# Kernel tuning notes

Hardware: AMD Instinct MI355X
Metric: run time of the kernel (lower is better)

The kernel has to match this reference:

```python
import jax, jax.numpy as jnp
import numpy as np

D_MODEL = 1024
N_HEAD = 16
D_K = D_MODEL // N_HEAD
B, S = 2, 2048
NEG = -1000000000.0


def setup_inputs() -> dict:
    key = jax.random.key(0)
    ks = jax.random.split(key, 9)
    inp = {
        "input_q": jax.random.normal(ks[0], (B, S, D_MODEL), dtype=jnp.float32),
        "input_k": jax.random.normal(ks[1], (B, S, D_MODEL), dtype=jnp.float32),
        "input_v": jax.random.normal(ks[2], (B, S, D_MODEL), dtype=jnp.float32),
        "mask": jax.random.randint(ks[3], (1, 1, S, S), 0, 2, dtype=jnp.int32),
        # parameters (Linear weights stored as [in, out] for x @ W)
        "w_q": jax.random.normal(ks[4], (D_MODEL, D_MODEL), dtype=jnp.float32) / np.sqrt(D_MODEL),
        "w_k": jax.random.normal(ks[5], (D_MODEL, D_MODEL), dtype=jnp.float32) / np.sqrt(D_MODEL),
        "w_v": jax.random.normal(ks[6], (D_MODEL, D_MODEL), dtype=jnp.float32) / np.sqrt(D_MODEL),
        "w_o": jax.random.normal(ks[7], (D_MODEL, D_MODEL), dtype=jnp.float32) / np.sqrt(D_MODEL),
        "b_o": jax.random.normal(ks[8], (D_MODEL,), dtype=jnp.float32) * 0.01,
    }
    return inp


def reference(input_q, input_k, input_v, mask, w_q, w_k, w_v, w_o, b_o):
    b = input_q.shape[0]
    # QKV projections -> [B, H, S, d_k]
    def split_heads(x):
        return x.reshape(b, -1, N_HEAD, D_K).transpose(0, 2, 1, 3)
    q = split_heads(input_q @ w_q)
    k = split_heads(input_k @ w_k)
    v = split_heads(input_v @ w_v)
    # naive attention: materialize [B, H, Sq, Sk] scores
    scores = jnp.einsum("bhqd,bhkd->bhqk", q, k) / jnp.sqrt(jnp.float32(D_K))
    scores = jnp.where(mask == 0, jnp.float32(NEG), scores)
    attn = jax.nn.softmax(scores, axis=-1)
    per_head = jnp.einsum("bhqk,bhkd->bhqd", attn, v)
    concat = per_head.transpose(0, 2, 1, 3).reshape(b, -1, N_HEAD * D_K)
    return concat @ w_o + b_o
```

## Files before the change

kernel.cpp:

```cpp
#include <hip/hip_runtime.h>
#include <hip/hip_bf16.h>

typedef _Float16 halfx8 __attribute__((ext_vector_type(8)));
typedef _Float16 halfx4 __attribute__((ext_vector_type(4)));
typedef _Float16 half2t __attribute__((ext_vector_type(2)));
typedef __fp16 fp16x2 __attribute__((ext_vector_type(2)));
typedef float floatx4 __attribute__((ext_vector_type(4)));

constexpr int S = 2048;
constexpr int DM = 1024;
constexpr int NH = 16;
constexpr int DK = 64;
constexpr int BATCH = 2;
constexpr int MROWS = 4096;
constexpr float QSCALE = 0.125f * 1.44269504088896340736f;

#if defined(__has_builtin)
#if __has_builtin(__builtin_amdgcn_fdot2)
#define HAVE_FDOT2 1
#endif
#endif

static __device__ inline half2t pack2(float a, float b) {
  return __builtin_bit_cast(half2t, __builtin_amdgcn_cvt_pkrtz(a, b));
}

static __device__ inline void load_lds16(const _Float16* g, _Float16* l) {
  __builtin_amdgcn_global_load_lds((const __attribute__((address_space(1))) void*)g,
                                   (__attribute__((address_space(3))) void*)l, 16, 0, 0);
}

__global__ void convert_w4(const float* __restrict__ w0, const float* __restrict__ w1,
                           const float* __restrict__ w2, const float* __restrict__ w3,
                           _Float16* __restrict__ o0, _Float16* __restrict__ o1,
                           _Float16* __restrict__ o2, _Float16* __restrict__ o3) {
  const float* w = (blockIdx.z == 0) ? w0 : (blockIdx.z == 1) ? w1 : (blockIdx.z == 2) ? w2 : w3;
  _Float16* wt = (blockIdx.z == 0) ? o0 : (blockIdx.z == 1) ? o1 : (blockIdx.z == 2) ? o2 : o3;
  __shared__ float tile[32][33];
  int n0 = blockIdx.x * 32, k0 = blockIdx.y * 32;
  int tx = threadIdx.x, ty = threadIdx.y;
#pragma unroll
  for (int i = 0; i < 4; ++i)
    tile[ty + i * 8][tx] = w[(k0 + ty + i * 8) * DM + n0 + tx];
  __syncthreads();
#pragma unroll
  for (int i = 0; i < 4; ++i)
    wt[(n0 + ty + i * 8) * DM + k0 + tx] = (_Float16)tile[tx][ty + i * 8];
}

__global__ void convert_in3(const float* __restrict__ a0, const float* __restrict__ a1,
                            const float* __restrict__ a2, _Float16* __restrict__ o0,
                            _Float16* __restrict__ o1, _Float16* __restrict__ o2) {
  const float* a = (blockIdx.z == 0) ? a0 : (blockIdx.z == 1) ? a1 : a2;
  _Float16* o = (blockIdx.z == 0) ? o0 : (blockIdx.z == 1) ? o1 : o2;
  size_t i = ((size_t)blockIdx.x * 256 + threadIdx.x) * 8;
  float4 va = *(const float4*)(a + i);
  float4 vb = *(const float4*)(a + i + 4);
  union { halfx8 v; _Float16 h[8]; } u;
  u.h[0] = (_Float16)va.x; u.h[1] = (_Float16)va.y;
  u.h[2] = (_Float16)va.z; u.h[3] = (_Float16)va.w;
  u.h[4] = (_Float16)vb.x; u.h[5] = (_Float16)vb.y;
  u.h[6] = (_Float16)vb.z; u.h[7] = (_Float16)vb.w;
  *(halfx8*)(o + i) = u.v;
}

__global__ void mask_swz(const int* __restrict__ m, _Float16* __restrict__ Mt) {
  int t = blockIdx.x * 256 + threadIdx.x;
  int j0 = (t & 1) * 8;
  int quad = (t >> 1) & 3;
  int q = (t >> 3) & (S - 1);
  int kt = t >> 14;
  const int* src = m + (size_t)q * S + kt * 64 + (j0 >> 2) * 16 + quad * 4;
  int4 a = *(const int4*)src;
  int4 b = *(const int4*)(src + 16);
  union { halfx8 v; _Float16 h[8]; } u;
  u.h[0] = (_Float16)(a.x != 0); u.h[1] = (_Float16)(a.y != 0);
  u.h[2] = (_Float16)(a.z != 0); u.h[3] = (_Float16)(a.w != 0);
  u.h[4] = (_Float16)(b.x != 0); u.h[5] = (_Float16)(b.y != 0);
  u.h[6] = (_Float16)(b.z != 0); u.h[7] = (_Float16)(b.w != 0);
  *(halfx8*)(Mt + (size_t)t * 8) = u.v;
}

__global__ __launch_bounds__(256) void qkv_gemm(const _Float16* __restrict__ xq,
                                                const _Float16* __restrict__ xk,
                                                const _Float16* __restrict__ xv,
                                                const _Float16* __restrict__ wqkv,
                                                _Float16* __restrict__ Qf,
                                                _Float16* __restrict__ Kf,
                                                _Float16* __restrict__ Vt) {
  __shared__ __align__(16) _Float16 smem[17408];
  _Float16* Asm = smem;
  _Float16* Bsm = smem + 128 * 64;
  const int tid = threadIdx.x;
  const int w = tid >> 6, l = tid & 63, lo = l & 15, quad = l >> 4;
  const int lo7 = l & 7;
  const int wm = (w >> 1) * 64, wn = (w & 1) * 64;
  const int bx = blockIdx.x, bm = blockIdx.y * 128;
  const int wid = bx >> 3;
  const _Float16* A = (wid == 0) ? xq : (wid == 1) ? xk : xv;
  const _Float16* Bt = wqkv + (size_t)bx * 128 * DM;

  floatx4 acc[4][4] = {};

  for (int k0 = 0; k0 < DM; k0 += 64) {
#pragma unroll
    for (int i = 0; i < 4; ++i) {
      int chunk = i * 256 + tid;
      int r = chunk >> 3;
      int c = (chunk & 7) ^ (r & 7);
      load_lds16(A + (size_t)(bm + r) * DM + k0 + c * 8, Asm + chunk * 8);
    }
#pragma unroll
    for (int i = 0; i < 4; ++i) {
      int chunk = i * 256 + tid;
      int r = chunk >> 3;
      int c = (chunk & 7) ^ (r & 7);
      load_lds16(Bt + (size_t)r * DM + k0 + c * 8, Bsm + chunk * 8);
    }
    __syncthreads();

#pragma unroll
    for (int ks = 0; ks < 2; ++ks) {
      halfx8 af[4], bf[4];
#pragma unroll
      for (int mt = 0; mt < 4; ++mt)
        af[mt] = *(const halfx8*)&Asm[(wm + mt * 16 + lo) * 64 + (((ks * 4 + quad) ^ lo7) * 8)];
#pragma unroll
      for (int nt = 0; nt < 4; ++nt)
        bf[nt] = *(const halfx8*)&Bsm[(wn + nt * 16 + lo) * 64 + (((ks * 4 + quad) ^ lo7) * 8)];
#pragma unroll
      for (int mt = 0; mt < 4; ++mt)
#pragma unroll
        for (int nt = 0; nt < 4; ++nt)
          acc[mt][nt] =
              __builtin_amdgcn_mfma_f32_16x16x32_f16(af[mt], bf[nt], acc[mt][nt], 0, 0, 0);
    }
    __syncthreads();
  }

  if (wid == 2) {
    constexpr int LDTT = 136;
    _Float16* tb = smem;
#pragma unroll
    for (int mt = 0; mt < 4; ++mt)
#pragma unroll
      for (int nt = 0; nt < 4; ++nt)
#pragma unroll
        for (int r = 0; r < 4; ++r) {
          int dl = wn + nt * 16 + lo;
          int sl = wm + mt * 16 + quad * 4 + r;
          tb[dl * LDTT + sl] = (_Float16)acc[mt][nt][r];
        }
    __syncthreads();
    const int b = bm >> 11, s0 = bm & (S - 1);
    const int d2 = tid >> 1, chunk = (tid & 1) * 64;
    const int dg = ((bx & 7) * 128 + d2);
    const int h = dg >> 6, dd = dg & 63;
    _Float16* O = Vt + ((size_t)(b * NH + h) * DK + dd) * S + s0 + chunk;
#pragma unroll
    for (int j = 0; j < 8; ++j)
      *(halfx8*)(O + j * 8) = *(const halfx8*)&tb[d2 * LDTT + chunk + j * 8];
    return;
  }

  _Float16* Out = (wid == 0) ? Qf : Kf;
  const float scale = (wid == 0) ? QSCALE : 1.0f;
#pragma unroll
  for (int mt = 0; mt < 4; ++mt)
#pragma unroll
    for (int nt = 0; nt < 4; ++nt)
#pragma unroll
      for (int r = 0; r < 4; ++r) {
        int row = bm + wm + mt * 16 + quad * 4 + r;
        int col = (bx & 7) * 128 + wn + nt * 16 + lo;
        Out[(size_t)row * DM + col] = (_Float16)(acc[mt][nt][r] * scale);
      }
}

__global__ __launch_bounds__(256) void attn_kernel(const _Float16* __restrict__ Qf,
                                                   const _Float16* __restrict__ Kf,
                                                   const _Float16* __restrict__ Vt,
                                                   const _Float16* __restrict__ Mt,
                                                   _Float16* __restrict__ concat) {
  __shared__ __align__(16) _Float16 Ksm[64 * 64];
  __shared__ __align__(16) _Float16 Vsm[64 * 64];
  __shared__ __align__(16) _Float16 Psm[4 * 16 * 64];

  const int tid = threadIdx.x;
  const int w = tid >> 6, l = tid & 63, lo = l & 15, quad = l >> 4;
  const int lo7 = l & 7;
  const int qb = blockIdx.x * 64 + w * 16;
  const int h = blockIdx.y, b = blockIdx.z;

  const _Float16* Vb = Vt + (size_t)(b * NH + h) * DK * S;
  const _Float16* Mw = Mt + ((size_t)(qb + lo) * 4 + quad) * 16;

  halfx8 qf[2];
#pragma unroll
  for (int ks = 0; ks < 2; ++ks)
    qf[ks] = *(const halfx8*)(Qf + ((size_t)b * S + qb + lo) * DM + h * DK + ks * 32 + quad * 8);

  floatx4 Oacc[4] = {};
  float lsum = 0.f;
  const half2t onev = {(_Float16)1.0f, (_Float16)1.0f};
  _Float16* Pw = &Psm[w * 16 * 64];

  for (int kt = 0; kt < S / 64; ++kt) {
#pragma unroll
    for (int i = 0; i < 2; ++i) {
      int chunk = i * 256 + tid;
      int r = chunk >> 3;
      int c = (chunk & 7) ^ (r & 7);
      load_lds16(Kf + ((size_t)b * S + kt * 64 + r) * DM + h * DK + c * 8, Ksm + chunk * 8);
      load_lds16(Vb + (size_t)r * S + kt * 64 + c * 8, Vsm + chunk * 8);
    }
    union { halfx8 v; half2t h2[4]; } m0, m1;
    m0.v = *(const halfx8*)(Mw + (size_t)kt * 131072);
    m1.v = *(const halfx8*)(Mw + (size_t)kt * 131072 + 8);
    __syncthreads();

    floatx4 Sacc[4] = {};
#pragma unroll
    for (int ks = 0; ks < 2; ++ks)
#pragma unroll
      for (int nt = 0; nt < 4; ++nt) {
        halfx8 kf = *(const halfx8*)&Ksm[(nt * 16 + lo) * 64 + (((ks * 4 + quad) ^ lo7) * 8)];
        Sacc[nt] = __builtin_amdgcn_mfma_f32_16x16x32_f16(kf, qf[ks], Sacc[nt], 0, 0, 0);
      }

    half2t mm[8];
    mm[0] = m0.h2[0]; mm[1] = m0.h2[1]; mm[2] = m0.h2[2]; mm[3] = m0.h2[3];
    mm[4] = m1.h2[0]; mm[5] = m1.h2[1]; mm[6] = m1.h2[2]; mm[7] = m1.h2[3];
#pragma unroll
    for (int nt = 0; nt < 4; ++nt) {
      half2t p01 = pack2(__builtin_exp2f(Sacc[nt][0]), __builtin_exp2f(Sacc[nt][1]));
      half2t p23 = pack2(__builtin_exp2f(Sacc[nt][2]), __builtin_exp2f(Sacc[nt][3]));
      p01 *= mm[nt * 2];
      p23 *= mm[nt * 2 + 1];
#ifdef HAVE_FDOT2
      lsum = __builtin_amdgcn_fdot2(__builtin_bit_cast(fp16x2, p01),
                                    __builtin_bit_cast(fp16x2, onev), lsum, false);
      lsum = __builtin_amdgcn_fdot2(__builtin_bit_cast(fp16x2, p23),
                                    __builtin_bit_cast(fp16x2, onev), lsum, false);
#else
      lsum += (float)p01[0] + (float)p01[1] + (float)p23[0] + (float)p23[1];
#endif
      union { halfx4 v; half2t h[2]; } u;
      u.h[0] = p01; u.h[1] = p23;
      *(halfx4*)&Pw[lo * 64 + (((2 * nt + (quad >> 1)) ^ lo7) * 8) + (quad & 1) * 4] = u.v;
    }

#pragma unroll
    for (int ks = 0; ks < 2; ++ks) {
      halfx8 pf = *(const halfx8*)&Pw[lo * 64 + (((ks * 4 + quad) ^ lo7) * 8)];
#pragma unroll
      for (int nt = 0; nt < 4; ++nt) {
        halfx8 vf = *(const halfx8*)&Vsm[(nt * 16 + lo) * 64 + (((ks * 4 + quad) ^ lo7) * 8)];
        Oacc[nt] = __builtin_amdgcn_mfma_f32_16x16x32_f16(pf, vf, Oacc[nt], 0, 0, 0);
      }
    }
    __syncthreads();
  }

  lsum += __shfl_xor(lsum, 16);
  lsum += __shfl_xor(lsum, 32);

#pragma unroll
  for (int r = 0; r < 4; ++r) {
    float lr = __shfl(lsum, quad * 4 + r);
    float inv = __builtin_amdgcn_rcpf(lr);
    int q = qb + quad * 4 + r;
#pragma unroll
    for (int nt = 0; nt < 4; ++nt) {
      int d = nt * 16 + lo;
      concat[((size_t)b * S + q) * DM + h * DK + d] = (_Float16)(Oacc[nt][r] * inv);
    }
  }
}

__global__ __launch_bounds__(256) void out_gemm(const _Float16* __restrict__ A,
                                                const _Float16* __restrict__ Bt,
                                                float* __restrict__ Cp,
                                                const float* __restrict__ bias) {
  __shared__ __align__(16) _Float16 Asm[128 * 64];
  __shared__ __align__(16) _Float16 Bsm[64 * 64];
  const int tid = threadIdx.x;
  const int w = tid >> 6, l = tid & 63, lo = l & 15, quad = l >> 4;
  const int lo7 = l & 7;
  const int wm = (w >> 1) * 64, wn = (w & 1) * 32;
  const int bm = blockIdx.y * 128, bn = blockIdx.x * 64;

  floatx4 acc[4][2] = {};

  for (int k0 = 0; k0 < DM; k0 += 64) {
#pragma unroll
    for (int i = 0; i < 4; ++i) {
      int chunk = i * 256 + tid;
      int r = chunk >> 3;
      int c = (chunk & 7) ^ (r & 7);
      load_lds16(A + (size_t)(bm + r) * DM + k0 + c * 8, Asm + chunk * 8);
    }
#pragma unroll
    for (int i = 0; i < 2; ++i) {
      int chunk = i * 256 + tid;
      int r = chunk >> 3;
      int c = (chunk & 7) ^ (r & 7);
      load_lds16(Bt + (size_t)(bn + r) * DM + k0 + c * 8, Bsm + chunk * 8);
    }
    __syncthreads();

#pragma unroll
    for (int ks = 0; ks < 2; ++ks) {
      halfx8 af[4], bfr[2];
#pragma unroll
      for (int mt = 0; mt < 4; ++mt)
        af[mt] = *(const halfx8*)&Asm[(wm + mt * 16 + lo) * 64 + (((ks * 4 + quad) ^ lo7) * 8)];
#pragma unroll
      for (int nt = 0; nt < 2; ++nt)
        bfr[nt] = *(const halfx8*)&Bsm[(wn + nt * 16 + lo) * 64 + (((ks * 4 + quad) ^ lo7) * 8)];
#pragma unroll
      for (int mt = 0; mt < 4; ++mt)
#pragma unroll
        for (int nt = 0; nt < 2; ++nt)
          acc[mt][nt] =
              __builtin_amdgcn_mfma_f32_16x16x32_f16(af[mt], bfr[nt], acc[mt][nt], 0, 0, 0);
    }
    __syncthreads();
  }

#pragma unroll
  for (int mt = 0; mt < 4; ++mt)
#pragma unroll
    for (int nt = 0; nt < 2; ++nt)
#pragma unroll
      for (int r = 0; r < 4; ++r) {
        int row = bm + wm + mt * 16 + quad * 4 + r;
        int col = bn + wn + nt * 16 + lo;
        Cp[(size_t)row * DM + col] = acc[mt][nt][r] + bias[col];
      }
}

extern "C" void kernel_launch(void* const* d_in, const int* in_sizes, int n_in,
                              void* d_out, int out_size, void* d_ws, size_t ws_size,
                              hipStream_t stream) {
  const float* in_q = (const float*)d_in[0];
  const float* in_k = (const float*)d_in[1];
  const float* in_v = (const float*)d_in[2];
  const int* mask = (const int*)d_in[3];
  const float* w_q = (const float*)d_in[4];
  const float* w_k = (const float*)d_in[5];
  const float* w_v = (const float*)d_in[6];
  const float* w_o = (const float*)d_in[7];
  const float* b_o = (const float*)d_in[8];
  float* out = (float*)d_out;

  char* ws = (char*)d_ws;
  constexpr size_t WB = (size_t)DM * DM * sizeof(_Float16);
  constexpr size_t MB_ = (size_t)S * S * sizeof(_Float16);
  constexpr size_t TB = (size_t)MROWS * DM * sizeof(_Float16);
  _Float16* wqkv = (_Float16*)(ws);
  _Float16* wto = (_Float16*)(ws + 3 * WB);
  _Float16* Mt = (_Float16*)(ws + 4 * WB);
  char* p = ws + 4 * WB + MB_;
  _Float16* Qf = (_Float16*)(p);
  _Float16* Kf = (_Float16*)(p + TB);
  _Float16* Vt = (_Float16*)(p + 2 * TB);
  _Float16* xq = (_Float16*)(p + 3 * TB);
  _Float16* xk = (_Float16*)(p + 4 * TB);
  _Float16* xv = (_Float16*)(p + 5 * TB);
  _Float16* concat = xq;

  convert_w4<<<dim3(32, 32, 4), dim3(32, 8), 0, stream>>>(
      w_q, w_k, w_v, w_o, wqkv, wqkv + DM * DM, wqkv + 2 * DM * DM, wto);
  convert_in3<<<dim3(MROWS * DM / 8 / 256, 1, 3), 256, 0, stream>>>(in_q, in_k, in_v,
                                                                    xq, xk, xv);
  mask_swz<<<dim3(S * S / 8 / 256), 256, 0, stream>>>(mask, Mt);

  qkv_gemm<<<dim3(24, 32), 256, 0, stream>>>(xq, xk, xv, wqkv, Qf, Kf, Vt);
  attn_kernel<<<dim3(S / 64, NH, BATCH), 256, 0, stream>>>(Qf, Kf, Vt, Mt, concat);
  out_gemm<<<dim3(DM / 64, MROWS / 128), 256, 0, stream>>>(concat, wto, out, b_o);
}
```

Baseline: 266.3 us.

## Double-buffer attention and output GEMM, widen attention tile to 32 rows per wave

Result: faster. 250.7 us (-5.8%).

```diff
diff --git a/kernel.cpp b/kernel.cpp
--- a/kernel.cpp
+++ b/kernel.cpp
@@ -19,10 +19,25 @@
 #if __has_builtin(__builtin_amdgcn_fdot2)
 #define HAVE_FDOT2 1
 #endif
+#if __has_builtin(__builtin_amdgcn_exp2f)
+#define EXP2F(x) __builtin_amdgcn_exp2f(x)
+#endif
+#endif
+#ifndef EXP2F
+#define EXP2F(x) __builtin_exp2f(x)
 #endif
 
 static __device__ inline half2t pack2(float a, float b) {
   return __builtin_bit_cast(half2t, __builtin_amdgcn_cvt_pkrtz(a, b));
+}
+
+static __device__ inline float hdot2(half2t a, half2t b, float c) {
+#ifdef HAVE_FDOT2
+  return __builtin_amdgcn_fdot2(__builtin_bit_cast(fp16x2, a),
+                                __builtin_bit_cast(fp16x2, b), c, false);
+#else
+  return c + (float)a[0] * (float)b[0] + (float)a[1] * (float)b[1];
+#endif
 }
 
 static __device__ inline void load_lds16(const _Float16* g, _Float16* l) {
@@ -177,166 +192,210 @@
       }
 }
 
-__global__ __launch_bounds__(256) void attn_kernel(const _Float16* __restrict__ Qf,
-                                                   const _Float16* __restrict__ Kf,
-                                                   const _Float16* __restrict__ Vt,
-                                                   const _Float16* __restrict__ Mt,
-                                                   _Float16* __restrict__ concat) {
-  __shared__ __align__(16) _Float16 Ksm[64 * 64];
-  __shared__ __align__(16) _Float16 Vsm[64 * 64];
-  __shared__ __align__(16) _Float16 Psm[4 * 16 * 64];
+__global__ __launch_bounds__(256, 2) void attn_kernel(const _Float16* __restrict__ Qf,
+                                                      const _Float16* __restrict__ Kf,
+                                                      const _Float16* __restrict__ Vt,
+                                                      const _Float16* __restrict__ Mt,
+                                                      _Float16* __restrict__ concat) {
+  __shared__ __align__(16) _Float16 K0s[64 * 64], K1s[64 * 64];
+  __shared__ __align__(16) _Float16 V0s[64 * 64], V1s[64 * 64];
+  __shared__ __align__(16) _Float16 Psm[4 * 32 * 64];
 
   const int tid = threadIdx.x;
-  const int w = tid >> 6, l = tid & 63, lo = l & 15, quad = l >> 4;
-  const int lo7 = l & 7;
-  const int qb = blockIdx.x * 64 + w * 16;
+  const int w = tid >> 6, l = tid & 63, lo = l & 15, quad = l >> 4, lo7 = l & 7;
+  const int qb = blockIdx.x * 128 + w * 32;
   const int h = blockIdx.y, b = blockIdx.z;
 
+  const _Float16* Kbase = Kf + (size_t)b * S * DM + h * DK;
   const _Float16* Vb = Vt + (size_t)(b * NH + h) * DK * S;
-  const _Float16* Mw = Mt + ((size_t)(qb + lo) * 4 + quad) * 16;
-
-  halfx8 qf[2];
-#pragma unroll
-  for (int ks = 0; ks < 2; ++ks)
-    qf[ks] = *(const halfx8*)(Qf + ((size_t)b * S + qb + lo) * DM + h * DK + ks * 32 + quad * 8);
-
-  floatx4 Oacc[4] = {};
-  float lsum = 0.f;
+  _Float16* Pw = Psm + w * 32 * 64;
+
+  const int r0 = tid >> 3, c0 = (tid & 7) ^ (r0 & 7);
+  const int r1 = (256 + tid) >> 3, c1 = ((256 + tid) & 7) ^ (r1 & 7);
+
+  halfx8 qf[2][2];
+  const _Float16* Mp[2];
+#pragma unroll
+  for (int g = 0; g < 2; ++g) {
+#pragma unroll
+    for (int ks = 0; ks < 2; ++ks)
+      qf[g][ks] = *(const halfx8*)(Qf + ((size_t)b * S + qb + g * 16 + lo) * DM + h * DK +
+                                   ks * 32 + quad * 8);
+    Mp[g] = Mt + ((size_t)(qb + g * 16 + lo) * 4 + quad) * 16;
+  }
+
+  floatx4 Oacc[2][4] = {};
+  float lsum[2] = {0.f, 0.f};
   const half2t onev = {(_Float16)1.0f, (_Float16)1.0f};
-  _Float16* Pw = &Psm[w * 16 * 64];
-
-  for (int kt = 0; kt < S / 64; ++kt) {
-#pragma unroll
-    for (int i = 0; i < 2; ++i) {
-      int chunk = i * 256 + tid;
-      int r = chunk >> 3;
-      int c = (chunk & 7) ^ (r & 7);
-      load_lds16(Kf + ((size_t)b * S + kt * 64 + r) * DM + h * DK + c * 8, Ksm + chunk * 8);
-      load_lds16(Vb + (size_t)r * S + kt * 64 + c * 8, Vsm + chunk * 8);
-    }
-    union { halfx8 v; half2t h2[4]; } m0, m1;
-    m0.v = *(const halfx8*)(Mw + (size_t)kt * 131072);
-    m1.v = *(const halfx8*)(Mw + (size_t)kt * 131072 + 8);
-    __syncthreads();
-
-    floatx4 Sacc[4] = {};
+
+  auto stage = [&](int kt, _Float16* Kd, _Float16* Vd) {
+    load_lds16(Kbase + (size_t)(kt * 64 + r0) * DM + c0 * 8, Kd + tid * 8);
+    load_lds16(Vb + (size_t)r0 * S + kt * 64 + c0 * 8, Vd + tid * 8);
+    load_lds16(Kbase + (size_t)(kt * 64 + r1) * DM + c1 * 8, Kd + (256 + tid) * 8);
+    load_lds16(Vb + (size_t)r1 * S + kt * 64 + c1 * 8, Vd + (256 + tid) * 8);
+  };
+
+  auto tile = [&](const _Float16* Kc, const _Float16* Vc, const halfx8* mc) {
+    floatx4 Sacc[2][4] = {};
 #pragma unroll
     for (int ks = 0; ks < 2; ++ks)
 #pragma unroll
       for (int nt = 0; nt < 4; ++nt) {
-        halfx8 kf = *(const halfx8*)&Ksm[(nt * 16 + lo) * 64 + (((ks * 4 + quad) ^ lo7) * 8)];
-        Sacc[nt] = __builtin_amdgcn_mfma_f32_16x16x32_f16(kf, qf[ks], Sacc[nt], 0, 0, 0);
-      }
-
-    half2t mm[8];
-    mm[0] = m0.h2[0]; mm[1] = m0.h2[1]; mm[2] = m0.h2[2]; mm[3] = m0.h2[3];
-    mm[4] = m1.h2[0]; mm[5] = m1.h2[1]; mm[6] = m1.h2[2]; mm[7] = m1.h2[3];
-#pragma unroll
-    for (int nt = 0; nt < 4; ++nt) {
-      half2t p01 = pack2(__builtin_exp2f(Sacc[nt][0]), __builtin_exp2f(Sacc[nt][1]));
-      half2t p23 = pack2(__builtin_exp2f(Sacc[nt][2]), __builtin_exp2f(Sacc[nt][3]));
-      p01 *= mm[nt * 2];
-      p23 *= mm[nt * 2 + 1];
-#ifdef HAVE_FDOT2
-      lsum = __builtin_amdgcn_fdot2(__builtin_bit_cast(fp16x2, p01),
-                                    __builtin_bit_cast(fp16x2, onev), lsum, false);
-      lsum = __builtin_amdgcn_fdot2(__builtin_bit_cast(fp16x2, p23),
-                                    __builtin_bit_cast(fp16x2, onev), lsum, false);
-#else
-      lsum += (float)p01[0] + (float)p01[1] + (float)p23[0] + (float)p23[1];
-#endif
-      union { halfx4 v; half2t h[2]; } u;
-      u.h[0] = p01; u.h[1] = p23;
-      *(halfx4*)&Pw[lo * 64 + (((2 * nt + (quad >> 1)) ^ lo7) * 8) + (quad & 1) * 4] = u.v;
-    }
-
+        halfx8 kf = *(const halfx8*)&Kc[(nt * 16 + lo) * 64 + (((ks * 4 + quad) ^ lo7) * 8)];
+        Sacc[0][nt] = __builtin_amdgcn_mfma_f32_16x16x32_f16(kf, qf[0][ks], Sacc[0][nt], 0, 0, 0);
+        Sacc[1][nt] = __builtin_amdgcn_mfma_f32_16x16x32_f16(kf, qf[1][ks], Sacc[1][nt], 0, 0, 0);
+      }
+#pragma unroll
+    for (int g = 0; g < 2; ++g) {
+      union { halfx8 v; half2t h2[4]; } mu0, mu1;
+      mu0.v = mc[g * 2];
+      mu1.v = mc[g * 2 + 1];
+      half2t mm[8] = {mu0.h2[0], mu0.h2[1], mu0.h2[2], mu0.h2[3],
+                      mu1.h2[0], mu1.h2[1], mu1.h2[2], mu1.h2[3]};
+#pragma unroll
+      for (int nt = 0; nt < 4; ++nt) {
+        half2t p01 = pack2(EXP2F(Sacc[g][nt][0]), EXP2F(Sacc[g][nt][1]));
+        half2t p23 = pack2(EXP2F(Sacc[g][nt][2]), EXP2F(Sacc[g][nt][3]));
+        p01 *= mm[nt * 2];
+        p23 *= mm[nt * 2 + 1];
+        lsum[g] = hdot2(p01, onev, lsum[g]);
+        lsum[g] = hdot2(p23, onev, lsum[g]);
+        union { halfx4 v; half2t hh[2]; } u;
+        u.hh[0] = p01;
+        u.hh[1] = p23;
+        *(halfx4*)&Pw[(g * 16 + lo) * 64 + (((2 * nt + (quad >> 1)) ^ lo7) * 8) +
+                      (quad & 1) * 4] = u.v;
+      }
+    }
 #pragma unroll
     for (int ks = 0; ks < 2; ++ks) {
-      halfx8 pf = *(const halfx8*)&Pw[lo * 64 + (((ks * 4 + quad) ^ lo7) * 8)];
+      halfx8 pf0 = *(const halfx8*)&Pw[lo * 64 + (((ks * 4 + quad) ^ lo7) * 8)];
+      halfx8 pf1 = *(const halfx8*)&Pw[(16 + lo) * 64 + (((ks * 4 + quad) ^ lo7) * 8)];
 #pragma unroll
       for (int nt = 0; nt < 4; ++nt) {
-        halfx8 vf = *(const halfx8*)&Vsm[(nt * 16 + lo) * 64 + (((ks * 4 + quad) ^ lo7) * 8)];
-        Oacc[nt] = __builtin_amdgcn_mfma_f32_16x16x32_f16(pf, vf, Oacc[nt], 0, 0, 0);
-      }
-    }
-    __syncthreads();
-  }
-
-  lsum += __shfl_xor(lsum, 16);
-  lsum += __shfl_xor(lsum, 32);
-
-#pragma unroll
-  for (int r = 0; r < 4; ++r) {
-    float lr = __shfl(lsum, quad * 4 + r);
-    float inv = __builtin_amdgcn_rcpf(lr);
-    int q = qb + quad * 4 + r;
-#pragma unroll
-    for (int nt = 0; nt < 4; ++nt) {
-      int d = nt * 16 + lo;
-      concat[((size_t)b * S + q) * DM + h * DK + d] = (_Float16)(Oacc[nt][r] * inv);
-    }
-  }
+        halfx8 vf = *(const halfx8*)&Vc[(nt * 16 + lo) * 64 + (((ks * 4 + quad) ^ lo7) * 8)];
+        Oacc[0][nt] = __builtin_amdgcn_mfma_f32_16x16x32_f16(pf0, vf, Oacc[0][nt], 0, 0, 0);
+        Oacc[1][nt] = __builtin_amdgcn_mfma_f32_16x16x32_f16(pf1, vf, Oacc[1][nt], 0, 0, 0);
+      }
+    }
+  };
+
+  halfx8 mr[4];
+#pragma unroll
+  for (int g = 0; g < 2; ++g) {
+    mr[g * 2] = *(const halfx8*)(Mp[g]);
+    mr[g * 2 + 1] = *(const halfx8*)(Mp[g] + 8);
+  }
+  stage(0, K0s, V0s);
+
+  for (int kt = 0; kt < S / 64; kt += 2) {
+    __syncthreads();
+    stage(kt + 1, K1s, V1s);
+    halfx8 mc[4] = {mr[0], mr[1], mr[2], mr[3]};
+#pragma unroll
+    for (int g = 0; g < 2; ++g) {
+      mr[g * 2] = *(const halfx8*)(Mp[g] + (size_t)(kt + 1) * 131072);
+      mr[g * 2 + 1] = *(const halfx8*)(Mp[g] + (size_t)(kt + 1) * 131072 + 8);
+    }
+    tile(K0s, V0s, mc);
+    __syncthreads();
+    if (kt + 2 < S / 64) stage(kt + 2, K0s, V0s);
+    mc[0] = mr[0]; mc[1] = mr[1]; mc[2] = mr[2]; mc[3] = mr[3];
+    if (kt + 2 < S / 64) {
+#pragma unroll
+      for (int g = 0; g < 2; ++g) {
+        mr[g * 2] = *(const halfx8*)(Mp[g] + (size_t)(kt + 2) * 131072);
+        mr[g * 2 + 1] = *(const halfx8*)(Mp[g] + (size_t)(kt + 2) * 131072 + 8);
+      }
+    }
+    tile(K1s, V1s, mc);
+  }
+
+#pragma unroll
+  for (int g = 0; g < 2; ++g) {
+    lsum[g] += __shfl_xor(lsum[g], 16);
+    lsum[g] += __shfl_xor(lsum[g], 32);
+  }
+
+#pragma unroll
+  for (int g = 0; g < 2; ++g)
+#pragma unroll
+    for (int r = 0; r < 4; ++r) {
+      float lr = __shfl(lsum[g], quad * 4 + r);
+      float inv = __builtin_amdgcn_rcpf(lr);
+      int q = qb + g * 16 + quad * 4 + r;
+#pragma unroll
+      for (int nt = 0; nt < 4; ++nt) {
+        int d = nt * 16 + lo;
+        concat[((size_t)b * S + q) * DM + h * DK + d] = (_Float16)(Oacc[g][nt][r] * inv);
+      }
+    }
 }
 
 __global__ __launch_bounds__(256) void out_gemm(const _Float16* __restrict__ A,
                                                 const _Float16* __restrict__ Bt,
                                                 float* __restrict__ Cp,
                                                 const float* __restrict__ bias) {
-  __shared__ __align__(16) _Float16 Asm[128 * 64];
-  __shared__ __align__(16) _Float16 Bsm[64 * 64];
+  __shared__ __align__(16) _Float16 A0s[128 * 64], A1s[128 * 64];
+  __shared__ __align__(16) _Float16 B0s[128 * 64], B1s[128 * 64];
   const int tid = threadIdx.x;
-  const int w = tid >> 6, l = tid & 63, lo = l & 15, quad = l >> 4;
-  const int lo7 = l & 7;
-  const int wm = (w >> 1) * 64, wn = (w & 1) * 32;
-  const int bm = blockIdx.y * 128, bn = blockIdx.x * 64;
-
-  floatx4 acc[4][2] = {};
-
-  for (int k0 = 0; k0 < DM; k0 += 64) {
+  const int w = tid >> 6, l = tid & 63, lo = l & 15, quad = l >> 4, lo7 = l & 7;
+  const int wm = (w >> 1) * 64, wn = (w & 1) * 64;
+  const int bm = blockIdx.y * 128, bn = blockIdx.x * 128;
+
+  floatx4 acc[4][4] = {};
+
+  auto stageg = [&](int k0, _Float16* Ad, _Float16* Bd) {
 #pragma unroll
     for (int i = 0; i < 4; ++i) {
       int chunk = i * 256 + tid;
-      int r = chunk >> 3;
-      int c = (chunk & 7) ^ (r & 7);
-      load_lds16(A + (size_t)(bm + r) * DM + k0 + c * 8, Asm + chunk * 8);
-    }
-#pragma unroll
-    for (int i = 0; i < 2; ++i) {
-      int chunk = i * 256 + tid;
-      int r = chunk >> 3;
-      int c = (chunk & 7) ^ (r & 7);
-      load_lds16(Bt + (size_t)(bn + r) * DM + k0 + c * 8, Bsm + chunk * 8);
-    }
-    __syncthreads();
-
+      int rr = chunk >> 3;
+      int cc = (chunk & 7) ^ (rr & 7);
+      load_lds16(A + (size_t)(bm + rr) * DM + k0 + cc * 8, Ad + chunk * 8);
+      load_lds16(Bt + (size_t)(bn + rr) * DM + k0 + cc * 8, Bd + chunk * 8);
+    }
+  };
+  auto comp = [&](const _Float16* As, const _Float16* Bs) {
 #pragma unroll
     for (int ks = 0; ks < 2; ++ks) {
-      halfx8 af[4], bfr[2];
+      halfx8 af[4], bf[4];
 #pragma unroll
       for (int mt = 0; mt < 4; ++mt)
-        af[mt] = *(const halfx8*)&Asm[(wm + mt * 16 + lo) * 64 + (((ks * 4 + quad) ^ lo7) * 8)];
-#pragma unroll
-      for (int nt = 0; nt < 2; ++nt)
-        bfr[nt] = *(const halfx8*)&Bsm[(wn + nt * 16 + lo) * 64 + (((ks * 4 + quad) ^ lo7) * 8)];
+        af[mt] = *(const halfx8*)&As[(wm + mt * 16 + lo) * 64 + (((ks * 4 + quad) ^ lo7) * 8)];
+#pragma unroll
+      for (int nt = 0; nt < 4; ++nt)
+        bf[nt] = *(const halfx8*)&Bs[(wn + nt * 16 + lo) * 64 + (((ks * 4 + quad) ^ lo7) * 8)];
 #pragma unroll
       for (int mt = 0; mt < 4; ++mt)
 #pragma unroll
-        for (int nt = 0; nt < 2; ++nt)
+        for (int nt = 0; nt < 4; ++nt)
           acc[mt][nt] =
-              __builtin_amdgcn_mfma_f32_16x16x32_f16(af[mt], bfr[nt], acc[mt][nt], 0, 0, 0);
-    }
-    __syncthreads();
-  }
-
+              __builtin_amdgcn_mfma_f32_16x16x32_f16(af[mt], bf[nt], acc[mt][nt], 0, 0, 0);
+    }
+  };
+
+  stageg(0, A0s, B0s);
+  for (int k0 = 0; k0 < DM; k0 += 128) {
+    __syncthreads();
+    stageg(k0 + 64, A1s, B1s);
+    comp(A0s, B0s);
+    __syncthreads();
+    if (k0 + 128 < DM) stageg(k0 + 128, A0s, B0s);
+    comp(A1s, B1s);
+  }
+
+  float bv[4];
+#pragma unroll
+  for (int nt = 0; nt < 4; ++nt) bv[nt] = bias[bn + wn + nt * 16 + lo];
 #pragma unroll
   for (int mt = 0; mt < 4; ++mt)
 #pragma unroll
-    for (int nt = 0; nt < 2; ++nt)
+    for (int nt = 0; nt < 4; ++nt)
 #pragma unroll
       for (int r = 0; r < 4; ++r) {
         int row = bm + wm + mt * 16 + quad * 4 + r;
         int col = bn + wn + nt * 16 + lo;
-        Cp[(size_t)row * DM + col] = acc[mt][nt][r] + bias[col];
+        Cp[(size_t)row * DM + col] = acc[mt][nt][r] + bv[nt];
       }
 }
 
@@ -377,6 +436,6 @@
   mask_swz<<<dim3(S * S / 8 / 256), 256, 0, stream>>>(mask, Mt);
 
   qkv_gemm<<<dim3(24, 32), 256, 0, stream>>>(xq, xk, xv, wqkv, Qf, Kf, Vt);
-  attn_kernel<<<dim3(S / 64, NH, BATCH), 256, 0, stream>>>(Qf, Kf, Vt, Mt, concat);
-  out_gemm<<<dim3(DM / 64, MROWS / 128), 256, 0, stream>>>(concat, wto, out, b_o);
-}
+  attn_kernel<<<dim3(S / 128, NH, BATCH), 256, 0, stream>>>(Qf, Kf, Vt, Mt, concat);
+  out_gemm<<<dim3(DM / 128, MROWS / 128), 256, 0, stream>>>(concat, wto, out, b_o);
+}
```
